# Performance work log

Hardware: AMD Instinct MI355X
Metric: run time of the kernel (lower is better)

Reference implementation:

```python
import jax, jax.numpy as jnp
import numpy as np

D = 256  # rst_input_dim


def _gru_cell(x, h, W_ih, W_hh, b_ih, b_hh):
    # x, h: (..., D); W_*: (3D, D); PyTorch GRU gate order: r, z, n
    gi = x @ W_ih.T + b_ih          # (..., 3D)
    gh = h @ W_hh.T + b_hh
    i_r, i_z, i_n = jnp.split(gi, 3, axis=-1)
    h_r, h_z, h_n = jnp.split(gh, 3, axis=-1)
    r = jax.nn.sigmoid(i_r + h_r)
    z = jax.nn.sigmoid(i_z + h_z)
    n = jnp.tanh(i_n + r * h_n)
    return (1.0 - z) * n + z * h


def setup_inputs() -> dict:
    key = jax.random.key(0)
    ks = jax.random.split(key, 5)
    B, L = 32, 4096
    s = 1.0 / np.sqrt(D)
    return {
        "leaf_embeds": jax.random.normal(ks[0], (B, L, D), dtype=jnp.float32),
        "W_ih": jax.random.normal(ks[1], (3 * D, D), dtype=jnp.float32) * s,
        "W_hh": jax.random.normal(ks[2], (3 * D, D), dtype=jnp.float32) * s,
        "b_ih": jax.random.normal(ks[3], (3 * D,), dtype=jnp.float32) * s,
        "b_hh": jax.random.normal(ks[4], (3 * D,), dtype=jnp.float32) * s,
    }


def reference(leaf_embeds, W_ih, W_hh, b_ih, b_hh):
    # Post-order traversal of a perfect binary tree, batched level-by-level
    # (classic tree-RNN same-depth batching). Leaves: embed = EDU embedding,
    # hidden = zeros. Internal node: h0 = mean(h_left, h_right); run GRU over
    # the 2-step sequence [left_embed, right_embed]; out = mean of the two
    # GRU outputs; returned hidden = final GRU hidden.
    embeds = leaf_embeds                      # (B, N, D)
    hs = jnp.zeros_like(leaf_embeds)          # (B, N, D)
    n = embeds.shape[1]
    while n > 1:
        xL, xR = embeds[:, 0::2], embeds[:, 1::2]   # (B, n/2, D)
        hL, hR = hs[:, 0::2], hs[:, 1::2]
        h0 = 0.5 * (hL + hR)                         # mean of child hiddens
        h1 = _gru_cell(xL, h0, W_ih, W_hh, b_ih, b_hh)
        h2 = _gru_cell(xR, h1, W_ih, W_hh, b_ih, b_hh)
        embeds = 0.5 * (h1 + h2)                     # mean over seq outputs
        hs = h2
        n //= 2
    return embeds[:, 0]                              # (B, D): root embedding
```

## Files before the change

kernel.cpp:

```cpp
#include <hip/hip_runtime.h>
#include <hip/hip_bf16.h>
#include <stdint.h>

typedef _Float16 f16x8 __attribute__((ext_vector_type(8)));
typedef _Float16 f16x4 __attribute__((ext_vector_type(4)));
typedef float    f32x4 __attribute__((ext_vector_type(4)));

#define GLDS16(gptr, lptr) \
  __builtin_amdgcn_global_load_lds((const __attribute__((address_space(1))) void*)(gptr), \
                                   (__attribute__((address_space(3))) void*)(lptr), 16, 0, 0)

#define WAITV(N) asm volatile("s_waitcnt vmcnt(" #N ")" ::: "memory")

__device__ __forceinline__ int tile_off(int rb, int c, int sub) {
    return ((rb * 4 + c) * 8 + sub) * 512;
}

__global__ __launch_bounds__(256) void prepack_weights(
    const float* __restrict__ Wih, const float* __restrict__ Whh,
    const float* __restrict__ bih, const float* __restrict__ bhh,
    _Float16* __restrict__ WP, float* __restrict__ BC)
{
    if (blockIdx.x == 2048) {
        int i = threadIdx.x;
        BC[i]       = bih[i] + bhh[i];
        BC[256 + i] = bih[256 + i] + bhh[256 + i];
        BC[512 + i] = bih[512 + i];
        BC[768 + i] = bhh[512 + i];
        return;
    }
    int idx = blockIdx.x * 256 + threadIdx.x;
    int j   = idx & 7;
    int nl  = (idx >> 3) & 63;
    int sub = (idx >> 9) & 7;
    int g   = (idx >> 12) & 3;
    int d0b = (idx >> 14) & 3;
    int c   = idx >> 16;
    int k = c * 64 + sub * 8 + j;
    int d = d0b * 64 + nl;
    float v = 0.f;
    if (g == 0)      v = (k < 256) ? Wih[d * 256 + k]         : Whh[d * 256 + (k - 256)];
    else if (g == 1) v = (k < 256) ? Wih[(256 + d) * 256 + k] : Whh[(256 + d) * 256 + (k - 256)];
    else if (g == 2) v = (k < 256) ? Wih[(512 + d) * 256 + k] : 0.f;
    else             v = (k >= 256) ? Whh[(512 + d) * 256 + (k - 256)] : 0.f;
    WP[idx] = (_Float16)v;
}

__global__ __launch_bounds__(256) void convert_split(
    const float* __restrict__ leaf, _Float16* __restrict__ XE, _Float16* __restrict__ XO)
{
    int g = blockIdx.x * 256 + threadIdx.x;
    int u = g & 31;
    int row = g >> 5;
    const float* src = leaf + (size_t)row * 256 + u * 8;
    float4 a = *(const float4*)src;
    float4 b = *(const float4*)(src + 4);
    f16x8 p;
    p[0] = (_Float16)a.x; p[1] = (_Float16)a.y; p[2] = (_Float16)a.z; p[3] = (_Float16)a.w;
    p[4] = (_Float16)b.x; p[5] = (_Float16)b.y; p[6] = (_Float16)b.z; p[7] = (_Float16)b.w;
    int ro = row >> 1;
    _Float16* dst = (row & 1) ? XO : XE;
    *(f16x8*)(dst + tile_off(ro >> 6, u >> 3, u & 7) + (ro & 63) * 8) = p;
}

template<int MT, bool SWIZ>
__global__ __launch_bounds__(256, 2) void gru_cell(
    const _Float16* __restrict__ Xsrc,
    const _Float16* __restrict__ Hsrc,
    const _Float16* __restrict__ WP,
    const float* __restrict__ BC,
    _Float16* __restrict__ Hout,
    _Float16* __restrict__ Ee, _Float16* __restrict__ Eo, _Float16* __restrict__ HP,
    int M)
{
    (void)M;
    constexpr int AROW = MT * 16 * 8;
    constexpr int ASZ  = 8 * AROW;
    __shared__ __align__(16) _Float16 Alds[2 * ASZ];

    const int tid  = threadIdx.x;
    int bm, d0b;
    if (SWIZ) {
        int xcd = blockIdx.x & 7, slot = blockIdx.x >> 3;
        d0b = slot & 3;
        bm  = (slot >> 2) * 8 + xcd;
    } else {
        bm = blockIdx.x >> 2; d0b = blockIdx.x & 3;
    }
    const int wave = tid >> 6, lane = tid & 63;
    const int quad = lane >> 4, lo = lane & 15;

    const bool has_h = (Hsrc != nullptr);
    const int nch = has_h ? 8 : 4;

    f32x4 acc[MT][4];
#pragma unroll
    for (int a = 0; a < MT; ++a)
#pragma unroll
        for (int b = 0; b < 4; ++b) acc[a][b] = (f32x4){0.f, 0.f, 0.f, 0.f};
    f16x4 hinvh[MT];

    auto loadB = [&](int c, f16x8 (&bb)[2][3]) {
        const size_t cb = (size_t)(c * 4 + d0b) * 4;
        const int col = (wave * 16 + lo) * 8;
#pragma unroll
        for (int ks = 0; ks < 2; ++ks) {
            const int subb = ks * 4 + quad;
#pragma unroll
            for (int slot = 0; slot < 3; ++slot) {
                int g = (slot == 2) ? ((c < 4) ? 2 : 3) : slot;
                bb[ks][slot] = *(const f16x8*)(WP + ((cb + g) * 8 + subb) * 512 + col);
            }
        }
    };

    auto issueA = [&](int c, int buf) {
        const _Float16* base = (c < 4) ? Xsrc : Hsrc;
        const int cc = c & 3;
        _Float16* Ab = Alds + buf * ASZ;
        constexpr int ND = MT / 2;
#pragma unroll
        for (int i = 0; i < ND; ++i) {
            int ai = wave * ND + i;
            int sub = ai >> 1, mh = ai & 1;
            GLDS16(base + tile_off(bm * (MT / 4) + mh, cc, sub) + lane * 8,
                   Ab + sub * AROW + mh * 512);
        }
    };

    auto compute = [&](int c, int buf, f16x8 (&bb)[2][3]) {
        const _Float16* Ab = Alds + buf * ASZ;
#pragma unroll
        for (int ks = 0; ks < 2; ++ks) {
            const int subb = ks * 4 + quad;
#pragma unroll
            for (int mt = 0; mt < MT; ++mt) {
                f16x8 a = *(const f16x8*)(Ab + subb * AROW + (mt * 16 + lo) * 8);
                acc[mt][0] = __builtin_amdgcn_mfma_f32_16x16x32_f16(a, bb[ks][0], acc[mt][0], 0, 0, 0);
                acc[mt][1] = __builtin_amdgcn_mfma_f32_16x16x32_f16(a, bb[ks][1], acc[mt][1], 0, 0, 0);
                if (c < 4)
                    acc[mt][2] = __builtin_amdgcn_mfma_f32_16x16x32_f16(a, bb[ks][2], acc[mt][2], 0, 0, 0);
                else
                    acc[mt][3] = __builtin_amdgcn_mfma_f32_16x16x32_f16(a, bb[ks][2], acc[mt][3], 0, 0, 0);
            }
        }
        if (has_h && c == 4 + d0b) {
            const int colw = wave * 16 + lo;
            const int sub = colw >> 3, j = colw & 7;
#pragma unroll
            for (int mt = 0; mt < MT; ++mt)
#pragma unroll
                for (int r = 0; r < 4; ++r)
                    hinvh[mt][r] = Ab[sub * AROW + (mt * 16 + quad * 4 + r) * 8 + j];
        }
    };

    issueA(0, 0);
    for (int c = 0; c < nch; ++c) {
        __syncthreads();
        f16x8 bb[2][3];
        loadB(c, bb);
        __builtin_amdgcn_sched_barrier(0);
        if (c + 1 < nch) issueA(c + 1, (c + 1) & 1);
        compute(c, c & 1, bb);
    }

    const int ld = wave * 16 + lo;
    const int d  = d0b * 64 + ld;
    const float brz0 = BC[d];
    const float brz1 = BC[256 + d];
    const float bni  = BC[512 + d];
    const float bnh  = BC[768 + d];
    constexpr int SROW = 72;
    constexpr int PR   = MT * 8;
    __syncthreads();
#pragma unroll
    for (int mt = 0; mt < MT; ++mt) {
        const int lr0 = mt * 16 + quad * 4;
        float hq[4];
#pragma unroll
        for (int r = 0; r < 4; ++r) {
            float hin = has_h ? (float)hinvh[mt][r] : 0.f;
            float rg = 1.f / (1.f + __expf(-(acc[mt][0][r] + brz0)));
            float zg = 1.f / (1.f + __expf(-(acc[mt][1][r] + brz1)));
            float ex = __expf(2.f * (acc[mt][2][r] + bni + rg * (acc[mt][3][r] + bnh)));
            float nv = 1.f - 2.f / (ex + 1.f);
            hq[r] = (1.f - zg) * nv + zg * hin;
            int lr = lr0 + r;
            if (Hout) {
                Alds[lr * SROW + ld] = (_Float16)hq[r];
            } else {
                Alds[(((lr & 1) * PR) + (lr >> 1)) * SROW + ld] =
                    (_Float16)(0.5f * (hin + hq[r]));
            }
        }
        if (!Hout) {
            Alds[(2 * PR + (lr0 >> 1)) * SROW + ld]     = (_Float16)(0.5f * (hq[0] + hq[1]));
            Alds[(2 * PR + (lr0 >> 1) + 1) * SROW + ld] = (_Float16)(0.5f * (hq[2] + hq[3]));
        }
    }
    __syncthreads();

    if (Hout) {
        constexpr int NU = MT * 128;
#pragma unroll
        for (int i = 0; i < NU / 256; ++i) {
            int uid = i * 256 + tid;
            int r = uid & 63, sub = (uid >> 6) & 7, mh = uid >> 9;
            f16x8 v = *(const f16x8*)&Alds[(mh * 64 + r) * SROW + sub * 8];
            *(f16x8*)(Hout + tile_off(bm * (MT / 4) + mh, d0b, sub) + r * 8) = v;
        }
    } else {
        constexpr int NU = 3 * PR * 8;
#pragma unroll
        for (int i = 0; i < NU / 256; ++i) {
            int uid = i * 256 + tid;
            int pr   = uid & (PR - 1);
            int rest = uid / PR;
            int sub = rest & 7, buf = rest >> 3;
            f16x8 v = *(const f16x8*)&Alds[(buf * PR + pr) * SROW + sub * 8];
            _Float16* dst = (buf == 0) ? Ee : (buf == 1) ? Eo : HP;
            *(f16x8*)(dst + tile_off(bm, d0b, sub) + pr * 8) = v;
        }
    }
}

__global__ __launch_bounds__(256, 1) void gru_tail16(
    const _Float16* __restrict__ Xe, const _Float16* __restrict__ Xo,
    const _Float16* __restrict__ HPs,
    const _Float16* __restrict__ WP, const float* __restrict__ BC,
    _Float16* __restrict__ Ee, _Float16* __restrict__ Eo,
    _Float16* __restrict__ HPd, float* __restrict__ out)
{
    __shared__ __align__(16) _Float16 A[3][1024];
    __shared__ __align__(16) _Float16 H1i[4][1024];

    const int tid  = threadIdx.x;
    const int wave = tid >> 6, lane = tid & 63;
    const int quad = lane >> 4, lo = lane & 15;
    const int bid  = blockIdx.x;
    const int m0 = bid * 16, rb = m0 >> 6, ro = m0 & 63;

    float brz0[4], brz1[4], bni[4], bnh[4];
#pragma unroll
    for (int nt = 0; nt < 4; ++nt) {
        int d = wave * 64 + nt * 16 + lo;
        brz0[nt] = BC[d];       brz1[nt] = BC[256 + d];
        bni[nt]  = BC[512 + d]; bnh[nt]  = BC[768 + d];
    }

    f32x4 acc[4][4];
    auto zacc = [&] {
#pragma unroll
        for (int nt = 0; nt < 4; ++nt)
#pragma unroll
            for (int g = 0; g < 4; ++g) acc[nt][g] = (f32x4){0.f, 0.f, 0.f, 0.f};
    };

    auto issueA = [&](const _Float16* base, int cc, int buf) {
        const int i = wave >> 1;
        GLDS16(base + tile_off(rb, cc, i * 4 + (lane >> 4)) + (ro + (lane & 15)) * 8,
               &A[buf][i * 512]);
    };

    auto loadB = [&](int c, f16x8 (&bb)[2][4][3]) {
#pragma unroll
        for (int ks = 0; ks < 2; ++ks) {
            const int subq = ks * 4 + quad;
            const _Float16* wb = WP + (size_t)((c * 4 + wave) * 4) * 4096 + subq * 512;
#pragma unroll
            for (int nt = 0; nt < 4; ++nt) {
                const int colb = (nt * 16 + lo) * 8;
                bb[ks][nt][0] = *(const f16x8*)(wb + colb);
                bb[ks][nt][1] = *(const f16x8*)(wb + 4096 + colb);
                bb[ks][nt][2] = *(const f16x8*)(wb + ((c < 4) ? 2 : 3) * 4096 + colb);
            }
        }
    };

    auto mfmaC = [&](int c, const _Float16* Ab, f16x8 (&bb)[2][4][3]) {
#pragma unroll
        for (int ks = 0; ks < 2; ++ks) {
            const int subq = ks * 4 + quad;
            f16x8 a = *(const f16x8*)(Ab + subq * 128 + lo * 8);
#pragma unroll
            for (int nt = 0; nt < 4; ++nt) {
                acc[nt][0] = __builtin_amdgcn_mfma_f32_16x16x32_f16(a, bb[ks][nt][0], acc[nt][0], 0, 0, 0);
                acc[nt][1] = __builtin_amdgcn_mfma_f32_16x16x32_f16(a, bb[ks][nt][1], acc[nt][1], 0, 0, 0);
                if (c < 4)
                    acc[nt][2] = __builtin_amdgcn_mfma_f32_16x16x32_f16(a, bb[ks][nt][2], acc[nt][2], 0, 0, 0);
                else
                    acc[nt][3] = __builtin_amdgcn_mfma_f32_16x16x32_f16(a, bb[ks][nt][2], acc[nt][3], 0, 0, 0);
            }
        }
    };

    zacc();
    float hin[4][4];
    issueA(Xe, 0, 0);
    issueA(Xe, 1, 1);
    for (int c = 0; c < 8; ++c) {
        if (c < 7) WAITV(1); else WAITV(0);
        __builtin_amdgcn_s_barrier();
        __builtin_amdgcn_sched_barrier(0);
        f16x8 bb[2][4][3];
        loadB(c, bb);
        __builtin_amdgcn_sched_barrier(0);
        if (c + 2 < 8) {
            int cn = c + 2;
            issueA((cn < 4) ? Xe : HPs, cn & 3, cn % 3);
        }
        const _Float16* Ab = A[c % 3];
        mfmaC(c, Ab, bb);
        if (c == 4 + wave) {
#pragma unroll
            for (int nt = 0; nt < 4; ++nt) {
                const int sb = nt * 2 + (lo >> 3), j = lo & 7;
#pragma unroll
                for (int r = 0; r < 4; ++r)
                    hin[nt][r] = (float)Ab[sb * 128 + (quad * 4 + r) * 8 + j];
            }
        }
    }

    __syncthreads();
    float h1v[4][4];
#pragma unroll
    for (int nt = 0; nt < 4; ++nt) {
        const int sb = nt * 2 + (lo >> 3), j = lo & 7;
#pragma unroll
        for (int r = 0; r < 4; ++r) {
            float rg = 1.f / (1.f + __expf(-(acc[nt][0][r] + brz0[nt])));
            float zg = 1.f / (1.f + __expf(-(acc[nt][1][r] + brz1[nt])));
            float ex = __expf(2.f * (acc[nt][2][r] + bni[nt] + rg * (acc[nt][3][r] + bnh[nt])));
            float nv = 1.f - 2.f / (ex + 1.f);
            float h  = (1.f - zg) * nv + zg * hin[nt][r];
            h1v[nt][r] = h;
            H1i[wave][sb * 128 + (quad * 4 + r) * 8 + j] = (_Float16)h;
        }
    }
    __syncthreads();

    zacc();
    issueA(Xo, 0, 0);
    issueA(Xo, 1, 1);
    for (int c = 0; c < 4; ++c) {
        if (c < 3) WAITV(1); else WAITV(0);
        __builtin_amdgcn_s_barrier();
        __builtin_amdgcn_sched_barrier(0);
        f16x8 bb[2][4][3];
        loadB(c, bb);
        __builtin_amdgcn_sched_barrier(0);
        if (c + 2 < 4) issueA(Xo, c + 2, (c + 2) % 3);
        mfmaC(c, A[c % 3], bb);
    }
#pragma unroll
    for (int c = 4; c < 8; ++c) {
        f16x8 bb[2][4][3];
        loadB(c, bb);
        mfmaC(c, &H1i[c - 4][0], bb);
    }

#pragma unroll
    for (int nt = 0; nt < 4; ++nt) {
        const int sb = nt * 2 + (lo >> 3), j = lo & 7;
        float h2[4];
#pragma unroll
        for (int r = 0; r < 4; ++r) {
            float rg = 1.f / (1.f + __expf(-(acc[nt][0][r] + brz0[nt])));
            float zg = 1.f / (1.f + __expf(-(acc[nt][1][r] + brz1[nt])));
            float ex = __expf(2.f * (acc[nt][2][r] + bni[nt] + rg * (acc[nt][3][r] + bnh[nt])));
            float nv = 1.f - 2.f / (ex + 1.f);
            h2[r] = (1.f - zg) * nv + zg * h1v[nt][r];
        }
        if (out) {
#pragma unroll
            for (int r = 0; r < 4; ++r)
                out[(size_t)(m0 + quad * 4 + r) * 256 + wave * 64 + nt * 16 + lo] =
                    0.5f * (h1v[nt][r] + h2[r]);
        } else {
            const int rbE   = bid >> 3;
            const int rbase = (bid & 7) * 8 + quad * 2;
            const int toff  = tile_off(rbE, wave, sb);
#pragma unroll
            for (int r = 0; r < 4; ++r) {
                _Float16* dst = (r & 1) ? Eo : Ee;
                dst[toff + (rbase + (r >> 1)) * 8 + j] =
                    (_Float16)(0.5f * (h1v[nt][r] + h2[r]));
            }
            HPd[toff + rbase * 8 + j]       = (_Float16)(0.5f * (h2[0] + h2[1]));
            HPd[toff + (rbase + 1) * 8 + j] = (_Float16)(0.5f * (h2[2] + h2[3]));
        }
    }
}

extern "C" void kernel_launch(void* const* d_in, const int* in_sizes, int n_in,
                              void* d_out, int out_size, void* d_ws, size_t ws_size,
                              hipStream_t stream) {
    const float* leaf = (const float*)d_in[0];
    const float* Wih  = (const float*)d_in[1];
    const float* Whh  = (const float*)d_in[2];
    const float* bih  = (const float*)d_in[3];
    const float* bhh  = (const float*)d_in[4];

    char* ws = (char*)d_ws;
    _Float16* WPp = (_Float16*)ws;
    _Float16* XAe = (_Float16*)(ws + (1ull  << 20));
    _Float16* XAo = (_Float16*)(ws + (33ull << 20));
    _Float16* XBe = (_Float16*)(ws + (65ull << 20));
    _Float16* XBo = (_Float16*)(ws + (81ull << 20));
    _Float16* H1  = (_Float16*)(ws + (97ull << 20));
    _Float16* HP2 = (_Float16*)(ws + (113ull << 20));
    _Float16* HPb = (_Float16*)(ws + (129ull << 20));
    float*    BCp = (float*)(ws + (145ull << 20));

    prepack_weights<<<2049, 256, 0, stream>>>(Wih, Whh, bih, bhh, WPp, BCp);
    convert_split<<<16384, 256, 0, stream>>>(leaf, XAe, XAo);

    _Float16 *XeC = XAe, *XoC = XAo, *XeN = XBe, *XoN = XBo;
    const _Float16* hp = nullptr;
    int M = 65536;
    for (int lev = 0; lev < 4; ++lev) {
        int grid = (M / 128) * 4;
        gru_cell<8, true><<<grid, 256, 0, stream>>>(XeC, hp, WPp, BCp,
                                                    H1, nullptr, nullptr, nullptr, M);
        gru_cell<8, true><<<grid, 256, 0, stream>>>(XoC, H1, WPp, BCp,
                                                    nullptr, XeN, XoN, HPb, M);
        hp = HPb;
        _Float16* t;
        t = XeC; XeC = XeN; XeN = t;
        t = XoC; XoC = XoN; XoN = t;
        M >>= 1;
    }

    for (int lev = 4; lev <= 11; ++lev) {
        int nb = (65536 >> lev) / 16;
        _Float16* Xe = (lev & 1) ? XBe : XAe;
        _Float16* Xo = (lev & 1) ? XBo : XAo;
        _Float16* De = (lev & 1) ? XAe : XBe;
        _Float16* Do = (lev & 1) ? XAo : XBo;
        _Float16* HPsrc = (lev & 1) ? HP2 : HPb;
        _Float16* HPdst = (lev & 1) ? HPb : HP2;
        float* op = (lev == 11) ? (float*)d_out : nullptr;
        gru_tail16<<<nb, 256, 0, stream>>>(Xe, Xo, HPsrc, WPp, BCp,
                                           De, Do, HPdst, op);
    }
}
```

Baseline: 751.1 us.

## Restructure tail GRU kernel to 64-row blocks with full LDS staging

The tail-level kernel now gives each block 64 rows instead of 16 and stages all of Xe, Xo and the parent hidden into a 128KB LDS buffer up front. It then loops over four 64-column output passes, with each wave covering 16 columns for all 64 rows, so every weight fragment is reused across four M-tiles. This cuts weight traffic per row but launches 4x fewer blocks, which leaves the small late levels with very little parallelism. It also drops the old async double-buffered A pipeline, and the large LDS allocation limits occupancy.

```diff
diff --git a/kernel.cpp b/kernel.cpp
--- a/kernel.cpp
+++ b/kernel.cpp
@@ -225,171 +225,160 @@
     }
 }
 
-__global__ __launch_bounds__(256, 1) void gru_tail16(
+__global__ __launch_bounds__(256, 1) void gru_tail_lvl(
     const _Float16* __restrict__ Xe, const _Float16* __restrict__ Xo,
     const _Float16* __restrict__ HPs,
     const _Float16* __restrict__ WP, const float* __restrict__ BC,
     _Float16* __restrict__ Ee, _Float16* __restrict__ Eo,
-    _Float16* __restrict__ HPd, float* __restrict__ out)
+    _Float16* __restrict__ HPd, float* __restrict__ out, int M)
 {
-    __shared__ __align__(16) _Float16 A[3][1024];
-    __shared__ __align__(16) _Float16 H1i[4][1024];
+    __shared__ __align__(16) _Float16 L[65536];
+    _Float16* AX  = L;
+    _Float16* AH  = L + 16384;
+    _Float16* AO  = L + 32768;
+    _Float16* H1I = L + 49152;
 
     const int tid  = threadIdx.x;
     const int wave = tid >> 6, lane = tid & 63;
     const int quad = lane >> 4, lo = lane & 15;
-    const int bid  = blockIdx.x;
-    const int m0 = bid * 16, rb = m0 >> 6, ro = m0 & 63;
-
-    float brz0[4], brz1[4], bni[4], bnh[4];
-#pragma unroll
-    for (int nt = 0; nt < 4; ++nt) {
-        int d = wave * 64 + nt * 16 + lo;
-        brz0[nt] = BC[d];       brz1[nt] = BC[256 + d];
-        bni[nt]  = BC[512 + d]; bnh[nt]  = BC[768 + d];
-    }
+    const int bm   = blockIdx.x;
+
+    {
+        const _Float16* bases[3] = { Xe, HPs, Xo };
+#pragma unroll
+        for (int i = 0; i < 24; ++i) {
+            int u = wave * 24 + i;
+            int reg = u >> 5, unit = u & 31;
+            int cc = unit >> 3, sub = unit & 7;
+            GLDS16(bases[reg] + tile_off(bm, cc, sub) + lane * 8,
+                   L + reg * 16384 + cc * 4096 + sub * 512 + lane * 8);
+        }
+    }
+    WAITV(0);
+    __syncthreads();
 
     f32x4 acc[4][4];
     auto zacc = [&] {
 #pragma unroll
-        for (int nt = 0; nt < 4; ++nt)
-#pragma unroll
-            for (int g = 0; g < 4; ++g) acc[nt][g] = (f32x4){0.f, 0.f, 0.f, 0.f};
+        for (int a = 0; a < 4; ++a)
+#pragma unroll
+            for (int b = 0; b < 4; ++b) acc[a][b] = (f32x4){0.f, 0.f, 0.f, 0.f};
     };
 
-    auto issueA = [&](const _Float16* base, int cc, int buf) {
-        const int i = wave >> 1;
-        GLDS16(base + tile_off(rb, cc, i * 4 + (lane >> 4)) + (ro + (lane & 15)) * 8,
-               &A[buf][i * 512]);
+    auto passMM = [&](const _Float16* A0, const _Float16* A1, int p) {
+        const int col = (wave * 16 + lo) * 8;
+#pragma unroll
+        for (int c = 0; c < 8; ++c) {
+            f16x8 bb[2][3];
+            const size_t cb = (size_t)(c * 4 + p) * 4;
+#pragma unroll
+            for (int ks = 0; ks < 2; ++ks) {
+                const int subb = ks * 4 + quad;
+#pragma unroll
+                for (int slot = 0; slot < 3; ++slot) {
+                    int g = (slot == 2) ? ((c < 4) ? 2 : 3) : slot;
+                    bb[ks][slot] = *(const f16x8*)(WP + ((cb + g) * 8 + subb) * 512 + col);
+                }
+            }
+            const _Float16* Ab = (c < 4) ? A0 + c * 4096 : A1 + (c - 4) * 4096;
+#pragma unroll
+            for (int ks = 0; ks < 2; ++ks) {
+                const int subb = ks * 4 + quad;
+#pragma unroll
+                for (int mt = 0; mt < 4; ++mt) {
+                    f16x8 a = *(const f16x8*)(Ab + subb * 512 + (mt * 16 + lo) * 8);
+                    acc[mt][0] = __builtin_amdgcn_mfma_f32_16x16x32_f16(a, bb[ks][0], acc[mt][0], 0, 0, 0);
+                    acc[mt][1] = __builtin_amdgcn_mfma_f32_16x16x32_f16(a, bb[ks][1], acc[mt][1], 0, 0, 0);
+                    if (c < 4)
+                        acc[mt][2] = __builtin_amdgcn_mfma_f32_16x16x32_f16(a, bb[ks][2], acc[mt][2], 0, 0, 0);
+                    else
+                        acc[mt][3] = __builtin_amdgcn_mfma_f32_16x16x32_f16(a, bb[ks][2], acc[mt][3], 0, 0, 0);
+                }
+            }
+        }
     };
 
-    auto loadB = [&](int c, f16x8 (&bb)[2][4][3]) {
-#pragma unroll
-        for (int ks = 0; ks < 2; ++ks) {
-            const int subq = ks * 4 + quad;
-            const _Float16* wb = WP + (size_t)((c * 4 + wave) * 4) * 4096 + subq * 512;
-#pragma unroll
-            for (int nt = 0; nt < 4; ++nt) {
-                const int colb = (nt * 16 + lo) * 8;
-                bb[ks][nt][0] = *(const f16x8*)(wb + colb);
-                bb[ks][nt][1] = *(const f16x8*)(wb + 4096 + colb);
-                bb[ks][nt][2] = *(const f16x8*)(wb + ((c < 4) ? 2 : 3) * 4096 + colb);
-            }
-        }
-    };
-
-    auto mfmaC = [&](int c, const _Float16* Ab, f16x8 (&bb)[2][4][3]) {
-#pragma unroll
-        for (int ks = 0; ks < 2; ++ks) {
-            const int subq = ks * 4 + quad;
-            f16x8 a = *(const f16x8*)(Ab + subq * 128 + lo * 8);
-#pragma unroll
-            for (int nt = 0; nt < 4; ++nt) {
-                acc[nt][0] = __builtin_amdgcn_mfma_f32_16x16x32_f16(a, bb[ks][nt][0], acc[nt][0], 0, 0, 0);
-                acc[nt][1] = __builtin_amdgcn_mfma_f32_16x16x32_f16(a, bb[ks][nt][1], acc[nt][1], 0, 0, 0);
-                if (c < 4)
-                    acc[nt][2] = __builtin_amdgcn_mfma_f32_16x16x32_f16(a, bb[ks][nt][2], acc[nt][2], 0, 0, 0);
-                else
-                    acc[nt][3] = __builtin_amdgcn_mfma_f32_16x16x32_f16(a, bb[ks][nt][2], acc[nt][3], 0, 0, 0);
-            }
-        }
-    };
-
-    zacc();
-    float hin[4][4];
-    issueA(Xe, 0, 0);
-    issueA(Xe, 1, 1);
-    for (int c = 0; c < 8; ++c) {
-        if (c < 7) WAITV(1); else WAITV(0);
-        __builtin_amdgcn_s_barrier();
-        __builtin_amdgcn_sched_barrier(0);
-        f16x8 bb[2][4][3];
-        loadB(c, bb);
-        __builtin_amdgcn_sched_barrier(0);
-        if (c + 2 < 8) {
-            int cn = c + 2;
-            issueA((cn < 4) ? Xe : HPs, cn & 3, cn % 3);
-        }
-        const _Float16* Ab = A[c % 3];
-        mfmaC(c, Ab, bb);
-        if (c == 4 + wave) {
-#pragma unroll
-            for (int nt = 0; nt < 4; ++nt) {
-                const int sb = nt * 2 + (lo >> 3), j = lo & 7;
-#pragma unroll
-                for (int r = 0; r < 4; ++r)
-                    hin[nt][r] = (float)Ab[sb * 128 + (quad * 4 + r) * 8 + j];
-            }
-        }
-    }
-
+    const int dl = wave * 16 + lo;
+    const int hoff = (dl >> 3) * 512 + (dl & 7);
+
+    for (int p = 0; p < 4; ++p) {
+        zacc();
+        passMM(AX, AH, p);
+        const int d = p * 64 + dl;
+        const float brz0 = BC[d], brz1 = BC[256 + d];
+        const float bni = BC[512 + d], bnh = BC[768 + d];
+#pragma unroll
+        for (int mt = 0; mt < 4; ++mt) {
+#pragma unroll
+            for (int r = 0; r < 4; ++r) {
+                int rr = mt * 16 + quad * 4 + r;
+                float hin = (float)AH[p * 4096 + hoff + rr * 8];
+                float rg = 1.f / (1.f + __expf(-(acc[mt][0][r] + brz0)));
+                float zg = 1.f / (1.f + __expf(-(acc[mt][1][r] + brz1)));
+                float ex = __expf(2.f * (acc[mt][2][r] + bni + rg * (acc[mt][3][r] + bnh)));
+                float nv = 1.f - 2.f / (ex + 1.f);
+                H1I[p * 4096 + hoff + rr * 8] =
+                    (_Float16)((1.f - zg) * nv + zg * hin);
+            }
+        }
+    }
     __syncthreads();
-    float h1v[4][4];
-#pragma unroll
-    for (int nt = 0; nt < 4; ++nt) {
-        const int sb = nt * 2 + (lo >> 3), j = lo & 7;
-#pragma unroll
-        for (int r = 0; r < 4; ++r) {
-            float rg = 1.f / (1.f + __expf(-(acc[nt][0][r] + brz0[nt])));
-            float zg = 1.f / (1.f + __expf(-(acc[nt][1][r] + brz1[nt])));
-            float ex = __expf(2.f * (acc[nt][2][r] + bni[nt] + rg * (acc[nt][3][r] + bnh[nt])));
-            float nv = 1.f - 2.f / (ex + 1.f);
-            float h  = (1.f - zg) * nv + zg * hin[nt][r];
-            h1v[nt][r] = h;
-            H1i[wave][sb * 128 + (quad * 4 + r) * 8 + j] = (_Float16)h;
-        }
-    }
-    __syncthreads();
-
-    zacc();
-    issueA(Xo, 0, 0);
-    issueA(Xo, 1, 1);
-    for (int c = 0; c < 4; ++c) {
-        if (c < 3) WAITV(1); else WAITV(0);
-        __builtin_amdgcn_s_barrier();
-        __builtin_amdgcn_sched_barrier(0);
-        f16x8 bb[2][4][3];
-        loadB(c, bb);
-        __builtin_amdgcn_sched_barrier(0);
-        if (c + 2 < 4) issueA(Xo, c + 2, (c + 2) % 3);
-        mfmaC(c, A[c % 3], bb);
-    }
-#pragma unroll
-    for (int c = 4; c < 8; ++c) {
-        f16x8 bb[2][4][3];
-        loadB(c, bb);
-        mfmaC(c, &H1i[c - 4][0], bb);
-    }
-
-#pragma unroll
-    for (int nt = 0; nt < 4; ++nt) {
-        const int sb = nt * 2 + (lo >> 3), j = lo & 7;
-        float h2[4];
-#pragma unroll
-        for (int r = 0; r < 4; ++r) {
-            float rg = 1.f / (1.f + __expf(-(acc[nt][0][r] + brz0[nt])));
-            float zg = 1.f / (1.f + __expf(-(acc[nt][1][r] + brz1[nt])));
-            float ex = __expf(2.f * (acc[nt][2][r] + bni[nt] + rg * (acc[nt][3][r] + bnh[nt])));
-            float nv = 1.f - 2.f / (ex + 1.f);
-            h2[r] = (1.f - zg) * nv + zg * h1v[nt][r];
-        }
-        if (out) {
-#pragma unroll
-            for (int r = 0; r < 4; ++r)
-                out[(size_t)(m0 + quad * 4 + r) * 256 + wave * 64 + nt * 16 + lo] =
-                    0.5f * (h1v[nt][r] + h2[r]);
-        } else {
-            const int rbE   = bid >> 3;
-            const int rbase = (bid & 7) * 8 + quad * 2;
-            const int toff  = tile_off(rbE, wave, sb);
+
+    constexpr int SROW = 72, PR = 32;
+    for (int p = 0; p < 4; ++p) {
+        zacc();
+        passMM(AO, H1I, p);
+        const int d = p * 64 + dl;
+        const float brz0 = BC[d], brz1 = BC[256 + d];
+        const float bni = BC[512 + d], bnh = BC[768 + d];
+        __syncthreads();
+#pragma unroll
+        for (int mt = 0; mt < 4; ++mt) {
+            const int lr0 = mt * 16 + quad * 4;
+            float h1q[4], hq[4];
 #pragma unroll
             for (int r = 0; r < 4; ++r) {
-                _Float16* dst = (r & 1) ? Eo : Ee;
-                dst[toff + (rbase + (r >> 1)) * 8 + j] =
-                    (_Float16)(0.5f * (h1v[nt][r] + h2[r]));
-            }
-            HPd[toff + rbase * 8 + j]       = (_Float16)(0.5f * (h2[0] + h2[1]));
-            HPd[toff + (rbase + 1) * 8 + j] = (_Float16)(0.5f * (h2[2] + h2[3]));
+                int rr = lr0 + r;
+                float h1 = (float)H1I[p * 4096 + hoff + rr * 8];
+                h1q[r] = h1;
+                float rg = 1.f / (1.f + __expf(-(acc[mt][0][r] + brz0)));
+                float zg = 1.f / (1.f + __expf(-(acc[mt][1][r] + brz1)));
+                float ex = __expf(2.f * (acc[mt][2][r] + bni + rg * (acc[mt][3][r] + bnh)));
+                float nv = 1.f - 2.f / (ex + 1.f);
+                hq[r] = (1.f - zg) * nv + zg * h1;
+            }
+            if (out) {
+#pragma unroll
+                for (int r = 0; r < 4; ++r) {
+                    int m = bm * 64 + lr0 + r;
+                    if (m < M)
+                        out[(size_t)m * 256 + d] = 0.5f * (h1q[r] + hq[r]);
+                }
+            } else {
+#pragma unroll
+                for (int r = 0; r < 4; ++r) {
+                    int lr = lr0 + r;
+                    AX[(((lr & 1) * PR) + (lr >> 1)) * SROW + dl] =
+                        (_Float16)(0.5f * (h1q[r] + hq[r]));
+                }
+                AX[(2 * PR + (lr0 >> 1)) * SROW + dl]     = (_Float16)(0.5f * (hq[0] + hq[1]));
+                AX[(2 * PR + (lr0 >> 1) + 1) * SROW + dl] = (_Float16)(0.5f * (hq[2] + hq[3]));
+            }
+        }
+        if (!out) {
+            __syncthreads();
+            const int rbE  = bm >> 1;
+            const int roff = (bm & 1) * 32;
+#pragma unroll
+            for (int i = 0; i < 3; ++i) {
+                int uid = i * 256 + tid;
+                int pr   = uid & (PR - 1);
+                int rest = uid / PR;
+                int sub = rest & 7, buf = rest >> 3;
+                f16x8 v = *(const f16x8*)&AX[(buf * PR + pr) * SROW + sub * 8];
+                _Float16* dst = (buf == 0) ? Ee : (buf == 1) ? Eo : HPd;
+                *(f16x8*)(dst + tile_off(rbE, p, sub) + (roff + pr) * 8) = v;
+            }
         }
     }
 }
@@ -434,7 +423,8 @@
     }
 
     for (int lev = 4; lev <= 11; ++lev) {
-        int nb = (65536 >> lev) / 16;
+        int Ml = 65536 >> lev;
+        int nb = (Ml + 63) >> 6;
         _Float16* Xe = (lev & 1) ? XBe : XAe;
         _Float16* Xo = (lev & 1) ? XBo : XAo;
         _Float16* De = (lev & 1) ? XAe : XBe;
@@ -442,7 +432,7 @@
         _Float16* HPsrc = (lev & 1) ? HP2 : HPb;
         _Float16* HPdst = (lev & 1) ? HPb : HP2;
         float* op = (lev == 11) ? (float*)d_out : nullptr;
-        gru_tail16<<<nb, 256, 0, stream>>>(Xe, Xo, HPsrc, WPp, BCp,
-                                           De, Do, HPdst, op);
-    }
-}
+        gru_tail_lvl<<<nb, 256, 0, stream>>>(Xe, Xo, HPsrc, WPp, BCp,
+                                             De, Do, HPdst, op, Ml);
+    }
+}
```

After: 976.1 us. 30.0% more time.
